# Kernel optimization log

Measured on AMD Instinct MI355X. Metric: run time of the kernel, lower is better.

## Reference

```python
import jax, jax.numpy as jnp
import numpy as np
import math

MODEL_DIM = 4096
NUM_EXPERTS = 64
NUM_TOKENS = 8192
CAPACITY_FACTOR = 1.0
MIN_CAPACITY = 4


def setup_inputs() -> dict:
    key = jax.random.key(0)
    k1, k2, k3 = jax.random.split(key, 3)
    x = jax.random.normal(k1, (NUM_TOKENS, MODEL_DIM), dtype=jnp.float32)
    wg_weight = jax.random.normal(k2, (NUM_EXPERTS, MODEL_DIM), dtype=jnp.float32) * (1.0 / math.sqrt(MODEL_DIM))
    uniform_noise = jax.random.uniform(k3, (NUM_TOKENS, NUM_EXPERTS), dtype=jnp.float32)
    return {"x": x, "wg_weight": wg_weight, "uniform_noise": uniform_noise}


def reference(x, wg_weight, uniform_noise):
    # gate projection in fp32 (torch module forces .float())
    logits = jnp.einsum('sd,ed->se', x.astype(jnp.float32), wg_weight.astype(jnp.float32))
    gates = jax.nn.softmax(logits, axis=1)  # [s, e]
    s, e = gates.shape
    capacity = max(math.ceil(s / e * CAPACITY_FACTOR), MIN_CAPACITY)  # static: 128

    indices1_s = jnp.argmax(gates, axis=1)                      # [s]
    mask1 = jax.nn.one_hot(indices1_s, e, dtype=jnp.int32)      # [s, e]
    exp_counts = jnp.sum(mask1, axis=0)                         # [e]

    # load-balancing aux loss
    me = jnp.mean(gates, axis=0)
    ce = jnp.mean(mask1.astype(jnp.float32), axis=0)
    l_aux = jnp.sum(me * ce) * e

    # random capacity selection: per-expert top-`capacity` tokens by uniform noise
    mask1_rand = mask1.astype(jnp.float32) * uniform_noise      # [s, e]
    _, top_idx = jax.lax.top_k(mask1_rand.T, capacity)          # [e, capacity] token ids
    sel = jnp.zeros((s, e), jnp.int32).at[top_idx, jnp.arange(e)[:, None]].set(1)
    new_mask1 = mask1 * sel                                     # [s, e]

    # capacity-slot assignment via cumsum
    locations1 = jnp.cumsum(new_mask1, axis=0) - 1              # [s, e]
    locations1_s = jnp.sum(locations1 * new_mask1, axis=1)      # [s]

    gates_masked = gates * new_mask1.astype(jnp.float32)        # [s, e]
    locations1_sc = jax.nn.one_hot(locations1_s, capacity, dtype=jnp.float32)  # [s, c]
    combine_weights = jnp.einsum('se,sc->sec', gates_masked, locations1_sc)     # [s, e, c]
    dispatch_mask = combine_weights.astype(bool)
    return l_aux, combine_weights, dispatch_mask, exp_counts
```

## Files before the change

### kernel.cpp

```cpp
#include <hip/hip_runtime.h>

#define S    8192
#define Dm   4096
#define E    64
#define CAP  128
#define CCH  32
#define KC   (Dm/CCH)
#define KSUB 16
#define XSTR 260
#define WSTR 68

#define CW_OFF 1
#define DM_OFF (1 + (size_t)S*E*CAP)
#define EC_OFF (1 + 2*(size_t)S*E*CAP)

__global__ __launch_bounds__(256, 4)
void k1_partial(const float* __restrict__ x, const float* __restrict__ wg,
                float* __restrict__ part) {
    __shared__ float xs[KSUB][XSTR];
    __shared__ float ws[KSUB][WSTR];
    const int tb  = blockIdx.x >> 5;
    const int c   = blockIdx.x & 31;
    const int tid = threadIdx.x;
    const int tt  = tid & 31;
    const int ee  = tid >> 5;
    const int k0  = c * KC;

    float acc[64];
    #pragma unroll
    for (int i = 0; i < 64; i++) acc[i] = 0.f;

    const int xr = tid >> 2;
    const int xc = tid & 3;
    const int we = tid >> 2;
    const int wk = (tid & 3) * 4;

    for (int su = 0; su < KC / KSUB; su++) {
        const int ks0 = k0 + su * KSUB;
        #pragma unroll
        for (int i = 0; i < 4; i++) {
            const int row = i * 64 + xr;
            const float4 v = *(const float4*)(x + (size_t)(tb*256 + row) * Dm + ks0 + xc*4);
            xs[xc*4+0][row] = v.x;
            xs[xc*4+1][row] = v.y;
            xs[xc*4+2][row] = v.z;
            xs[xc*4+3][row] = v.w;
        }
        {
            const float4 v = *(const float4*)(wg + (size_t)we * Dm + ks0 + wk);
            ws[wk+0][we] = v.x; ws[wk+1][we] = v.y;
            ws[wk+2][we] = v.z; ws[wk+3][we] = v.w;
        }
        __syncthreads();
        #pragma unroll 4
        for (int kk = 0; kk < KSUB; kk++) {
            const float4 a0 = *(const float4*)&xs[kk][tt*8];
            const float4 a1 = *(const float4*)&xs[kk][tt*8+4];
            const float4 w0 = *(const float4*)&ws[kk][ee*8];
            const float4 w1 = *(const float4*)&ws[kk][ee*8+4];
            const float av[8] = {a0.x,a0.y,a0.z,a0.w,a1.x,a1.y,a1.z,a1.w};
            const float wv[8] = {w0.x,w0.y,w0.z,w0.w,w1.x,w1.y,w1.z,w1.w};
            #pragma unroll
            for (int t = 0; t < 8; t++)
                #pragma unroll
                for (int e = 0; e < 8; e++)
                    acc[t*8+e] = fmaf(av[t], wv[e], acc[t*8+e]);
        }
        __syncthreads();
    }
    #pragma unroll
    for (int t = 0; t < 8; t++) {
        float* dst = part + ((size_t)c * S + tb*256 + tt*8 + t) * E + ee*8;
        *(float4*)(dst)     = make_float4(acc[t*8+0], acc[t*8+1], acc[t*8+2], acc[t*8+3]);
        *(float4*)(dst + 4) = make_float4(acc[t*8+4], acc[t*8+5], acc[t*8+6], acc[t*8+7]);
    }
}

__global__ __launch_bounds__(256, 1)
void k1b_softmax(const float* __restrict__ part, float* __restrict__ gate_val,
                 int* __restrict__ idx1, int* __restrict__ counts,
                 float* __restrict__ me_sum) {
    const int tid = threadIdx.x, wv = tid >> 6, ln = tid & 63;
    const int token = blockIdx.x * 4 + wv;
    float p = 0.f;
    #pragma unroll
    for (int c = 0; c < CCH; c++) p += part[((size_t)c * S + token) * E + ln];
    float v = p; int i = ln;
    #pragma unroll
    for (int off = 1; off < 64; off <<= 1) {
        float ov = __shfl_xor(v, off, 64);
        int   oi = __shfl_xor(i, off, 64);
        if (ov > v || (ov == v && oi < i)) { v = ov; i = oi; }
    }
    float g = __expf(p - v);
    float ssum = g;
    #pragma unroll
    for (int off = 1; off < 64; off <<= 1) ssum += __shfl_xor(ssum, off, 64);
    const float gate = g / ssum;
    __shared__ float gs[4][64];
    gs[wv][ln] = gate;
    __syncthreads();
    if (tid < 64)
        atomicAdd(&me_sum[tid], gs[0][tid] + gs[1][tid] + gs[2][tid] + gs[3][tid]);
    if (ln == 0) {
        gate_val[token] = 1.0f / ssum;
        idx1[token] = i;
        atomicAdd(&counts[i], 1);
    }
}

__device__ __forceinline__ int block_reduce_sum(int v, int* tmp4, int tid) {
    #pragma unroll
    for (int off = 1; off < 64; off <<= 1) v += __shfl_xor(v, off, 64);
    __syncthreads();
    if ((tid & 63) == 0) tmp4[tid >> 6] = v;
    __syncthreads();
    return tmp4[0] + tmp4[1] + tmp4[2] + tmp4[3];
}

__device__ __forceinline__ int block_scan_incl(int val, int* a, int* b, int tid, int* total) {
    __syncthreads();
    a[tid] = val;
    __syncthreads();
    int* src = a; int* dst = b;
    #pragma unroll
    for (int off = 1; off < 256; off <<= 1) {
        int v = src[tid];
        if (tid >= off) v += src[tid - off];
        dst[tid] = v;
        __syncthreads();
        int* t = src; src = dst; dst = t;
    }
    *total = src[255];
    return src[tid];
}

__global__ __launch_bounds__(256, 1)
void k2_select(const int* __restrict__ idx1, const float* __restrict__ gate_val,
               const float* __restrict__ noise, const int* __restrict__ counts,
               const float* __restrict__ me_sum, float* __restrict__ out) {
    const int e = blockIdx.x;
    const int tid = threadIdx.x;
    __shared__ int idx_s[S];
    __shared__ unsigned short l_tok[S];
    __shared__ float l_ns[S];
    __shared__ int sa[256], sb[256];
    __shared__ int tmp4[4];

    for (int i = tid; i < S; i += 256) idx_s[i] = idx1[i];
    __syncthreads();

    int cnt = 0;
    #pragma unroll
    for (int j4 = 0; j4 < 8; j4++) {
        const int4 q = *(const int4*)&idx_s[tid * 32 + j4 * 4];
        cnt += (q.x == e) + (q.y == e) + (q.z == e) + (q.w == e);
    }
    int total_n;
    int incl = block_scan_incl(cnt, sa, sb, tid, &total_n);
    int pos = incl - cnt;
    const int n = total_n;
    #pragma unroll
    for (int j4 = 0; j4 < 8; j4++) {
        const int4 q = *(const int4*)&idx_s[tid * 32 + j4 * 4];
        const int qv[4] = {q.x, q.y, q.z, q.w};
        #pragma unroll
        for (int u = 0; u < 4; u++) {
            const int s = tid * 32 + j4 * 4 + u;
            if (qv[u] == e) {
                l_tok[pos] = (unsigned short)s;
                l_ns[pos]  = noise[(size_t)s * E + e];
                pos++;
            }
        }
    }
    __syncthreads();

    if (tid == 0) out[EC_OFF + e] = (float)n;

    unsigned int V = 0u;
    if (n > CAP) {
        unsigned int lo = 0u, hi = 0x3F800000u;
        while (hi - lo > 1u) {
            const unsigned int mid = (lo + hi) >> 1;
            int c = 0;
            for (int i2 = tid; i2 < n; i2 += 256)
                c += (__float_as_uint(l_ns[i2]) >= mid);
            const int cge = block_reduce_sum(c, tmp4, tid);
            if (cge >= CAP) lo = mid; else hi = mid;
        }
        V = lo;
    }

    const int m = (n + 255) >> 8;
    const int i_begin = min(n, tid * m);
    const int i_end   = min(n, i_begin + m);
    int gt_l = 0, eq_l = 0;
    for (int i2 = i_begin; i2 < i_end; i2++) {
        const unsigned int b = __float_as_uint(l_ns[i2]);
        gt_l += (b > V); eq_l += (b == V);
    }
    int tot_gt, tot_eq;
    const int incl_gt = block_scan_incl(gt_l, sa, sb, tid, &tot_gt);
    (void)incl_gt;
    const int incl_eq = block_scan_incl(eq_l, sa, sb, tid, &tot_eq);
    const int eq_excl = incl_eq - eq_l;
    const int take_eq = CAP - tot_gt;
    const int sel_l = gt_l + max(0, min(eq_l, take_eq - eq_excl));
    int tot_sel;
    const int incl_sel = block_scan_incl(sel_l, sa, sb, tid, &tot_sel);
    int slot = incl_sel - sel_l;
    int eq_seen = eq_excl;
    for (int i2 = i_begin; i2 < i_end; i2++) {
        const unsigned int b = __float_as_uint(l_ns[i2]);
        bool sel;
        if (b > V) sel = true;
        else if (b == V) { sel = (eq_seen < take_eq); eq_seen++; }
        else sel = false;
        if (sel) {
            const int tok = l_tok[i2];
            const float g = gate_val[tok];
            const size_t off = (size_t)tok * (E * CAP) + (size_t)e * CAP + slot;
            out[CW_OFF + off] = g;
            out[DM_OFF + off] = 1.0f;
            slot++;
        }
    }

    if (e == 0 && tid < 64) {
        float la = (me_sum[tid] / (float)S) * ((float)counts[tid] / (float)S);
        #pragma unroll
        for (int off = 1; off < 64; off <<= 1) la += __shfl_xor(la, off, 64);
        if (tid == 0) out[0] = la * (float)E;
    }
}

extern "C" void kernel_launch(void* const* d_in, const int* in_sizes, int n_in,
                              void* d_out, int out_size, void* d_ws, size_t ws_size,
                              hipStream_t stream) {
    const float* x     = (const float*)d_in[0];
    const float* wg    = (const float*)d_in[1];
    const float* noise = (const float*)d_in[2];
    float* out = (float*)d_out;
    float* ws  = (float*)d_ws;

    float* gate_val = ws;
    int*   idx1     = (int*)(ws + 8192);
    int*   counts   = (int*)(ws + 16384);
    float* me_sum   = ws + 16448;
    float* part     = ws + 16512;

    hipMemsetAsync(counts, 0, 128 * sizeof(int), stream);
    hipMemsetAsync(out, 0, (size_t)out_size * sizeof(float), stream);
    k1_partial  <<<dim3(1024), dim3(256), 0, stream>>>(x, wg, part);
    k1b_softmax <<<dim3(S/4),  dim3(256), 0, stream>>>(part, gate_val, idx1, counts, me_sum);
    k2_select   <<<dim3(E),    dim3(256), 0, stream>>>(idx1, gate_val, noise, counts, me_sum, out);
}
```

Measured before the change: 715.5 us.

## Replace output memset and scatter with single fill pass; retile gate GEMM

The full-output memset followed by scattered writes is replaced by a new fill kernel. k2_select now records only each token's selected slot position, and the fill kernel writes every output element exactly once (zero, or the gate and 1.0 at that slot). The gate GEMM is also retiled: the K split drops from 32 to 8 chunks to cut partial-sum traffic, each block covers 128 tokens, and the next K slice is prefetched into registers. The aim is to remove a redundant pass over the large output and reduce intermediate memory traffic. In exchange, the GEMM has fewer blocks and less parallelism, and the fill kernel uses scalar stores.

```diff
diff --git a/kernel.cpp b/kernel.cpp
--- a/kernel.cpp
+++ b/kernel.cpp
@@ -4,10 +4,11 @@
 #define Dm   4096
 #define E    64
 #define CAP  128
-#define CCH  32
+#define CCH  8
 #define KC   (Dm/CCH)
 #define KSUB 16
-#define XSTR 260
+#define TB   128
+#define XSTR 132
 #define WSTR 68
 
 #define CW_OFF 1
@@ -18,50 +19,53 @@
 void k1_partial(const float* __restrict__ x, const float* __restrict__ wg,
                 float* __restrict__ part) {
     __shared__ float xs[KSUB][XSTR];
-    __shared__ float ws[KSUB][WSTR];
-    const int tb  = blockIdx.x >> 5;
-    const int c   = blockIdx.x & 31;
+    __shared__ float wsh[KSUB][WSTR];
+    const int tb  = blockIdx.x >> 3;
+    const int c   = blockIdx.x & 7;
     const int tid = threadIdx.x;
-    const int tt  = tid & 31;
+    const int tg  = tid & 31;
     const int ee  = tid >> 5;
     const int k0  = c * KC;
 
-    float acc[64];
-    #pragma unroll
-    for (int i = 0; i < 64; i++) acc[i] = 0.f;
-
-    const int xr = tid >> 2;
-    const int xc = tid & 3;
-    const int we = tid >> 2;
-    const int wk = (tid & 3) * 4;
+    float acc[32];
+    #pragma unroll
+    for (int i = 0; i < 32; i++) acc[i] = 0.f;
+
+    const int xrow = tid >> 2;
+    const int xcol = tid & 3;
+    const int we   = tid >> 2;
+    const int wk   = (tid & 3) * 4;
+
+    const float* xp0 = x  + (size_t)(tb*TB + xrow)      * Dm + k0 + xcol*4;
+    const float* xp1 = x  + (size_t)(tb*TB + xrow + 64) * Dm + k0 + xcol*4;
+    const float* wp  = wg + (size_t)we * Dm + k0 + wk;
+
+    float4 va0 = *(const float4*)xp0;
+    float4 va1 = *(const float4*)xp1;
+    float4 vw  = *(const float4*)wp;
 
     for (int su = 0; su < KC / KSUB; su++) {
-        const int ks0 = k0 + su * KSUB;
-        #pragma unroll
-        for (int i = 0; i < 4; i++) {
-            const int row = i * 64 + xr;
-            const float4 v = *(const float4*)(x + (size_t)(tb*256 + row) * Dm + ks0 + xc*4);
-            xs[xc*4+0][row] = v.x;
-            xs[xc*4+1][row] = v.y;
-            xs[xc*4+2][row] = v.z;
-            xs[xc*4+3][row] = v.w;
-        }
-        {
-            const float4 v = *(const float4*)(wg + (size_t)we * Dm + ks0 + wk);
-            ws[wk+0][we] = v.x; ws[wk+1][we] = v.y;
-            ws[wk+2][we] = v.z; ws[wk+3][we] = v.w;
-        }
+        xs[xcol*4+0][xrow]    = va0.x; xs[xcol*4+1][xrow]    = va0.y;
+        xs[xcol*4+2][xrow]    = va0.z; xs[xcol*4+3][xrow]    = va0.w;
+        xs[xcol*4+0][xrow+64] = va1.x; xs[xcol*4+1][xrow+64] = va1.y;
+        xs[xcol*4+2][xrow+64] = va1.z; xs[xcol*4+3][xrow+64] = va1.w;
+        wsh[wk+0][we] = vw.x; wsh[wk+1][we] = vw.y;
+        wsh[wk+2][we] = vw.z; wsh[wk+3][we] = vw.w;
         __syncthreads();
-        #pragma unroll 4
+        if (su < KC/KSUB - 1) {
+            va0 = *(const float4*)(xp0 + (su+1)*KSUB);
+            va1 = *(const float4*)(xp1 + (su+1)*KSUB);
+            vw  = *(const float4*)(wp  + (su+1)*KSUB);
+        }
+        #pragma unroll
         for (int kk = 0; kk < KSUB; kk++) {
-            const float4 a0 = *(const float4*)&xs[kk][tt*8];
-            const float4 a1 = *(const float4*)&xs[kk][tt*8+4];
-            const float4 w0 = *(const float4*)&ws[kk][ee*8];
-            const float4 w1 = *(const float4*)&ws[kk][ee*8+4];
-            const float av[8] = {a0.x,a0.y,a0.z,a0.w,a1.x,a1.y,a1.z,a1.w};
+            const float4 a  = *(const float4*)&xs[kk][tg*4];
+            const float4 w0 = *(const float4*)&wsh[kk][ee*8];
+            const float4 w1 = *(const float4*)&wsh[kk][ee*8+4];
+            const float av[4] = {a.x, a.y, a.z, a.w};
             const float wv[8] = {w0.x,w0.y,w0.z,w0.w,w1.x,w1.y,w1.z,w1.w};
             #pragma unroll
-            for (int t = 0; t < 8; t++)
+            for (int t = 0; t < 4; t++)
                 #pragma unroll
                 for (int e = 0; e < 8; e++)
                     acc[t*8+e] = fmaf(av[t], wv[e], acc[t*8+e]);
@@ -69,8 +73,8 @@
         __syncthreads();
     }
     #pragma unroll
-    for (int t = 0; t < 8; t++) {
-        float* dst = part + ((size_t)c * S + tb*256 + tt*8 + t) * E + ee*8;
+    for (int t = 0; t < 4; t++) {
+        float* dst = part + ((size_t)c * S + tb*TB + tg*4 + t) * E + ee*8;
         *(float4*)(dst)     = make_float4(acc[t*8+0], acc[t*8+1], acc[t*8+2], acc[t*8+3]);
         *(float4*)(dst + 4) = make_float4(acc[t*8+4], acc[t*8+5], acc[t*8+6], acc[t*8+7]);
     }
@@ -136,9 +140,9 @@
 }
 
 __global__ __launch_bounds__(256, 1)
-void k2_select(const int* __restrict__ idx1, const float* __restrict__ gate_val,
-               const float* __restrict__ noise, const int* __restrict__ counts,
-               const float* __restrict__ me_sum, float* __restrict__ out) {
+void k2_select(const int* __restrict__ idx1, const float* __restrict__ noise,
+               const int* __restrict__ counts, const float* __restrict__ me_sum,
+               int* __restrict__ sel_pos, float* __restrict__ out) {
     const int e = blockIdx.x;
     const int tid = threadIdx.x;
     __shared__ int idx_s[S];
@@ -217,14 +221,9 @@
         if (b > V) sel = true;
         else if (b == V) { sel = (eq_seen < take_eq); eq_seen++; }
         else sel = false;
-        if (sel) {
-            const int tok = l_tok[i2];
-            const float g = gate_val[tok];
-            const size_t off = (size_t)tok * (E * CAP) + (size_t)e * CAP + slot;
-            out[CW_OFF + off] = g;
-            out[DM_OFF + off] = 1.0f;
-            slot++;
-        }
+        const int tok = l_tok[i2];
+        if (sel) { sel_pos[tok] = e * CAP + slot; slot++; }
+        else     { sel_pos[tok] = -1; }
     }
 
     if (e == 0 && tid < 64) {
@@ -232,6 +231,31 @@
         #pragma unroll
         for (int off = 1; off < 64; off <<= 1) la += __shfl_xor(la, off, 64);
         if (tid == 0) out[0] = la * (float)E;
+    }
+}
+
+__global__ __launch_bounds__(256)
+void k3_fill(const int* __restrict__ sel_pos, const float* __restrict__ gate_val,
+             float* __restrict__ out) {
+    const int tid  = threadIdx.x;
+    const int tok0 = blockIdx.x * 4;
+    #pragma unroll
+    for (int t = 0; t < 4; t++) {
+        const int tok = tok0 + t;
+        const int pos = sel_pos[tok];
+        const float g = gate_val[tok];
+        float* cw = out + CW_OFF + (size_t)tok * (E * CAP);
+        float* dm = cw + (size_t)S * (E * CAP);
+        #pragma unroll
+        for (int j = 0; j < 8; j++) {
+            const int b = j * 1024 + tid;
+            #pragma unroll
+            for (int q = 0; q < 4; q++) {
+                const int idx = b + q * 256;
+                cw[idx] = (idx == pos) ? g   : 0.f;
+                dm[idx] = (idx == pos) ? 1.f : 0.f;
+            }
+        }
     }
 }
 
@@ -248,11 +272,12 @@
     int*   idx1     = (int*)(ws + 8192);
     int*   counts   = (int*)(ws + 16384);
     float* me_sum   = ws + 16448;
-    float* part     = ws + 16512;
+    int*   sel_pos  = (int*)(ws + 16512);
+    float* part     = ws + 24704;
 
     hipMemsetAsync(counts, 0, 128 * sizeof(int), stream);
-    hipMemsetAsync(out, 0, (size_t)out_size * sizeof(float), stream);
-    k1_partial  <<<dim3(1024), dim3(256), 0, stream>>>(x, wg, part);
+    k1_partial  <<<dim3(512),  dim3(256), 0, stream>>>(x, wg, part);
     k1b_softmax <<<dim3(S/4),  dim3(256), 0, stream>>>(part, gate_val, idx1, counts, me_sum);
-    k2_select   <<<dim3(E),    dim3(256), 0, stream>>>(idx1, gate_val, noise, counts, me_sum, out);
-}
+    k2_select   <<<dim3(E),    dim3(256), 0, stream>>>(idx1, noise, counts, me_sum, sel_pos, out);
+    k3_fill     <<<dim3(S/4),  dim3(256), 0, stream>>>(sel_pos, gate_val, out);
+}
```

After: 736.0 us. +2.9%, slower.
